# Kernel tuning notes

Hardware: AMD Instinct MI355X
Metric: run time of the kernel (lower is better)

Reference implementation:

```python
import jax, jax.numpy as jnp
import numpy as np

N_A = 500000
N_B = 500000
NUM_HERBS = 25000
D = 128  # hidden_dim


def setup_inputs() -> dict:
    key = jax.random.key(0)
    ks = jax.random.split(key, 12)
    h_A = jax.random.normal(ks[0], (N_A, D), dtype=jnp.float32)
    h_B = jax.random.normal(ks[1], (N_B, D), dtype=jnp.float32)
    herb_idx_A = jnp.sort(jax.random.randint(ks[2], (N_A,), 0, NUM_HERBS, dtype=jnp.int64))
    herb_idx_B = jnp.sort(jax.random.randint(ks[3], (N_B,), 0, NUM_HERBS, dtype=jnp.int64))
    # attn_net: Linear(2D, D//2) -> LeakyReLU(0.2) -> Linear(D//2, 1)
    aw1 = jax.random.normal(ks[4], (2 * D, D // 2), dtype=jnp.float32) / np.sqrt(2 * D)
    ab1 = jnp.zeros((D // 2,), dtype=jnp.float32)
    aw2 = jax.random.normal(ks[5], (D // 2, 1), dtype=jnp.float32) / np.sqrt(D // 2)
    ab2 = jnp.zeros((1,), dtype=jnp.float32)
    # fusion_mlp: Linear(4D, 2D) -> ReLU -> Linear(2D, D)
    fw1 = jax.random.normal(ks[6], (4 * D, 2 * D), dtype=jnp.float32) / np.sqrt(4 * D)
    fb1 = jnp.zeros((2 * D,), dtype=jnp.float32)
    fw2 = jax.random.normal(ks[7], (2 * D, D), dtype=jnp.float32) / np.sqrt(2 * D)
    fb2 = jnp.zeros((D,), dtype=jnp.float32)
    return {"h_A": h_A, "h_B": h_B, "herb_idx_A": herb_idx_A, "herb_idx_B": herb_idx_B,
            "num_herbs": NUM_HERBS,
            "aw1": aw1, "ab1": ab1, "aw2": aw2, "ab2": ab2,
            "fw1": fw1, "fb1": fb1, "fw2": fw2, "fb2": fb2}


def _seg_mean(x, idx, n):
    s = jax.ops.segment_sum(x, idx, num_segments=n)          # [n, D]
    cnt = jax.ops.segment_sum(jnp.ones((x.shape[0], 1), x.dtype), idx, num_segments=n)
    return s / jnp.maximum(cnt, 1.0)


def _seg_softmax(score, idx, n):
    # score: [N, 1]; numerically-stable per-segment softmax (as in PyG softmax)
    m = jax.ops.segment_max(score, idx, num_segments=n)       # [n, 1]
    e = jnp.exp(score - m[idx])
    denom = jax.ops.segment_sum(e, idx, num_segments=n)
    return e / (denom[idx] + 1e-16)


def _attn(x, aw1, ab1, aw2, ab2):
    h = jax.nn.leaky_relu(x @ aw1 + ab1, negative_slope=0.2)
    return h @ aw2 + ab2                                      # [N, 1]


def reference(h_A, h_B, herb_idx_A, herb_idx_B, num_herbs,
              aw1, ab1, aw2, ab2, fw1, fb1, fw2, fb2):
    H_B_mean = _seg_mean(h_B, herb_idx_B, num_herbs)          # [H, D]
    H_A_mean = _seg_mean(h_A, herb_idx_A, num_herbs)          # [H, D]

    cat_A = jnp.concatenate([h_A, H_B_mean[herb_idx_A]], axis=-1)  # [N_A, 2D]
    alpha_A = _seg_softmax(_attn(cat_A, aw1, ab1, aw2, ab2), herb_idx_A, num_herbs)
    H_A_given_B = jax.ops.segment_sum(alpha_A * h_A, herb_idx_A, num_segments=num_herbs)

    cat_B = jnp.concatenate([h_B, H_A_mean[herb_idx_B]], axis=-1)  # [N_B, 2D]
    alpha_B = _seg_softmax(_attn(cat_B, aw1, ab1, aw2, ab2), herb_idx_B, num_herbs)
    H_B_given_A = jax.ops.segment_sum(alpha_B * h_B, herb_idx_B, num_segments=num_herbs)

    concat_feat = jnp.concatenate([H_A_given_B, H_B_given_A,
                                   H_A_given_B * H_B_given_A,
                                   jnp.abs(H_A_given_B - H_B_given_A)], axis=-1)  # [H, 4D]
    H_interaction = jax.nn.relu(concat_feat @ fw1 + fb1) @ fw2 + fb2              # [H, D]
    return (H_interaction, H_A_given_B, H_B_given_A)
```

## Files before the change

kernel.cpp:

```cpp
#include <hip/hip_runtime.h>
#include <math.h>

#define H_HERBS 25000
#define DIM 128

typedef __attribute__((ext_vector_type(8))) short bf16x8;
typedef __attribute__((ext_vector_type(4))) float f32x4;

__device__ inline unsigned pack2bf(float a, float b) {
    union { float f; unsigned u; } x, y; x.f = a; y.f = b;
    return ((x.u + 0x8000u) >> 16) | ((y.u + 0x8000u) & 0xFFFF0000u);
}

__global__ void k_starts(const int* __restrict__ idxA, const int* __restrict__ idxB,
                         int nA, int nB, int* __restrict__ startA, int* __restrict__ startB) {
    int h = blockIdx.x * blockDim.x + threadIdx.x;
    if (h > H_HERBS) return;
    {
        int lo = 0, hi = nA;
        while (lo < hi) { int mid = (lo + hi) >> 1; if (idxA[mid] < h) lo = mid + 1; else hi = mid; }
        startA[h] = lo;
    }
    {
        int lo = 0, hi = nB;
        while (lo < hi) { int mid = (lo + hi) >> 1; if (idxB[mid] < h) lo = mid + 1; else hi = mid; }
        startB[h] = lo;
    }
}

__global__ __launch_bounds__(64) void k_packw(
        const float* __restrict__ fw1, const float* __restrict__ fw2,
        uint4* __restrict__ w1bf, uint4* __restrict__ w2bf) {
    int b = blockIdx.x, l = threadIdx.x;
    int c = l & 15, kg = l >> 4;
    if (b < 256) {
        int kt = b >> 4, nt = b & 15;
        int k0 = kt * 32 + kg * 8, j = nt * 16 + c;
        unsigned u0 = pack2bf(fw1[(size_t)(k0 + 0) * 256 + j], fw1[(size_t)(k0 + 1) * 256 + j]);
        unsigned u1 = pack2bf(fw1[(size_t)(k0 + 2) * 256 + j], fw1[(size_t)(k0 + 3) * 256 + j]);
        unsigned u2 = pack2bf(fw1[(size_t)(k0 + 4) * 256 + j], fw1[(size_t)(k0 + 5) * 256 + j]);
        unsigned u3 = pack2bf(fw1[(size_t)(k0 + 6) * 256 + j], fw1[(size_t)(k0 + 7) * 256 + j]);
        w1bf[(size_t)b * 64 + l] = make_uint4(u0, u1, u2, u3);
    } else {
        int bb = b - 256;
        int kt = bb >> 3, nt = bb & 7;
        int k0 = kt * 32 + kg * 8, j = nt * 16 + c;
        unsigned u0 = pack2bf(fw2[(size_t)(k0 + 0) * 128 + j], fw2[(size_t)(k0 + 1) * 128 + j]);
        unsigned u1 = pack2bf(fw2[(size_t)(k0 + 2) * 128 + j], fw2[(size_t)(k0 + 3) * 128 + j]);
        unsigned u2 = pack2bf(fw2[(size_t)(k0 + 4) * 128 + j], fw2[(size_t)(k0 + 5) * 128 + j]);
        unsigned u3 = pack2bf(fw2[(size_t)(k0 + 6) * 128 + j], fw2[(size_t)(k0 + 7) * 128 + j]);
        w2bf[(size_t)bb * 64 + l] = make_uint4(u0, u1, u2, u3);
    }
}

__global__ __launch_bounds__(256) void k_mean_both(
        const float* __restrict__ hA, const float* __restrict__ hB,
        const int* __restrict__ startA, const int* __restrict__ startB,
        const float* __restrict__ aw1, const float* __restrict__ ab1,
        float* __restrict__ mpartA, float* __restrict__ mpartB, int nhb) {
    __shared__ float Wl[128 * 64];
    __shared__ __align__(16) float mb[16][128];
    bool isA = (int)blockIdx.x < nhb;
    int hb = isA ? blockIdx.x : blockIdx.x - nhb;
    const float* X = isA ? hB : hA;
    const int* start = isA ? startB : startA;
    float* mpart = isA ? mpartA : mpartB;
    int h0 = hb * 16;
    int t = threadIdx.x;

    {
        const float4* Wsrc = (const float4*)(aw1 + 128 * 64);
        float4* Wl4 = (float4*)Wl;
        #pragma unroll
        for (int q = 0; q < 8; ++q) Wl4[t + 256 * q] = Wsrc[t + 256 * q];
    }

    int wv = t >> 6, ln = t & 63, half = ln >> 5, li = ln & 31;
    const float4* X4 = (const float4*)X;
    #pragma unroll
    for (int i = 0; i < 4; ++i) {
        int hh = wv * 4 + i;
        int h = h0 + hh;
        if (h >= H_HERBS) { if (half == 0) ((float4*)mb[hh])[li] = make_float4(0.f,0.f,0.f,0.f); continue; }
        int s = start[h], e = start[h + 1];
        float4 acc = make_float4(0.f, 0.f, 0.f, 0.f);
        int r = s + half;
        for (; r + 6 < e; r += 8) {
            float4 v0 = X4[(size_t)r * 32 + li];
            float4 v1 = X4[(size_t)(r + 2) * 32 + li];
            float4 v2 = X4[(size_t)(r + 4) * 32 + li];
            float4 v3 = X4[(size_t)(r + 6) * 32 + li];
            acc.x += (v0.x + v1.x) + (v2.x + v3.x);
            acc.y += (v0.y + v1.y) + (v2.y + v3.y);
            acc.z += (v0.z + v1.z) + (v2.z + v3.z);
            acc.w += (v0.w + v1.w) + (v2.w + v3.w);
        }
        for (; r < e; r += 2) {
            float4 v0 = X4[(size_t)r * 32 + li];
            acc.x += v0.x; acc.y += v0.y; acc.z += v0.z; acc.w += v0.w;
        }
        acc.x += __shfl_xor(acc.x, 32, 64);
        acc.y += __shfl_xor(acc.y, 32, 64);
        acc.z += __shfl_xor(acc.z, 32, 64);
        acc.w += __shfl_xor(acc.w, 32, 64);
        int cnt = e - s;
        float inv = 1.0f / (float)(cnt > 1 ? cnt : 1);
        if (half == 0) {
            ((float4*)mb[hh])[li] = make_float4(acc.x * inv, acc.y * inv, acc.z * inv, acc.w * inv);
        }
    }
    __syncthreads();

    {
        int j = t & 63, wg = t >> 6;
        float b1 = ab1[j];
        float a0 = b1, a1 = b1, a2 = b1, a3 = b1;
        #pragma unroll 8
        for (int k = 0; k < 128; ++k) {
            float w = Wl[k * 64 + j];
            a0 += mb[wg * 4 + 0][k] * w;
            a1 += mb[wg * 4 + 1][k] * w;
            a2 += mb[wg * 4 + 2][k] * w;
            a3 += mb[wg * 4 + 3][k] * w;
        }
        int h = h0 + wg * 4;
        if (h + 0 < H_HERBS) mpart[(size_t)(h + 0) * 64 + j] = a0;
        if (h + 1 < H_HERBS) mpart[(size_t)(h + 1) * 64 + j] = a1;
        if (h + 2 < H_HERBS) mpart[(size_t)(h + 2) * 64 + j] = a2;
        if (h + 3 < H_HERBS) mpart[(size_t)(h + 3) * 64 + j] = a3;
    }
}

__global__ __launch_bounds__(256) void k_scores_mfma(
        const float* __restrict__ XA, const int* __restrict__ idxA,
        const float* __restrict__ mpartA, int nA, int gridA,
        const float* __restrict__ XB, const int* __restrict__ idxB,
        const float* __restrict__ mpartB, int nB,
        const float* __restrict__ aw1, const float* __restrict__ aw2,
        const float* __restrict__ ab2,
        float* __restrict__ scoresA, float* __restrict__ scoresB) {
    bool isA = (int)blockIdx.x < gridA;
    int blk = isA ? blockIdx.x : blockIdx.x - gridA;
    const float* X = isA ? XA : XB;
    const int* idx = isA ? idxA : idxB;
    const float* mpart = isA ? mpartA : mpartB;
    float* scores = isA ? scoresA : scoresB;
    int n = isA ? nA : nB;

    int t = threadIdx.x;
    int l = t & 63, wid = t >> 6;
    int c = l & 15, kg = l >> 4;

    union ABu { bf16x8 v; unsigned u[4]; };

    ABu wf[4][4];
    #pragma unroll
    for (int kb = 0; kb < 4; ++kb) {
        int k0 = kb * 32 + kg * 8;
        #pragma unroll
        for (int nb = 0; nb < 4; ++nb) {
            int j = nb * 16 + c;
            #pragma unroll
            for (int e = 0; e < 4; ++e) {
                wf[kb][nb].u[e] = pack2bf(aw1[(size_t)(k0 + 2 * e)     * 64 + j],
                                          aw1[(size_t)(k0 + 2 * e + 1) * 64 + j]);
            }
        }
    }
    float a2[4];
    #pragma unroll
    for (int nb = 0; nb < 4; ++nb) a2[nb] = aw2[nb * 16 + c];
    float b2s = ab2[0];

    for (int pass = 0; pass < 4; ++pass) {
        long r0 = (long)blk * 256 + pass * 64 + wid * 16;
        if (r0 >= n) break;
        long myrow = r0 + c;
        if (myrow >= n) myrow = n - 1;
        const float4* Xr = (const float4*)(X + (size_t)myrow * DIM);

        ABu af[4];
        #pragma unroll
        for (int kb = 0; kb < 4; ++kb) {
            float4 a = Xr[kb * 8 + kg * 2];
            float4 b = Xr[kb * 8 + kg * 2 + 1];
            af[kb].u[0] = pack2bf(a.x, a.y);
            af[kb].u[1] = pack2bf(a.z, a.w);
            af[kb].u[2] = pack2bf(b.x, b.y);
            af[kb].u[3] = pack2bf(b.z, b.w);
        }

        f32x4 acc[4];
        #pragma unroll
        for (int nb = 0; nb < 4; ++nb) { acc[nb].x = 0.f; acc[nb].y = 0.f; acc[nb].z = 0.f; acc[nb].w = 0.f; }
        #pragma unroll
        for (int kb = 0; kb < 4; ++kb) {
            #pragma unroll
            for (int nb = 0; nb < 4; ++nb) {
                acc[nb] = __builtin_amdgcn_mfma_f32_16x16x32_bf16(af[kb].v, wf[kb][nb].v, acc[nb], 0, 0, 0);
            }
        }

        int rgrp = kg * 4;
        float part[4] = {0.f, 0.f, 0.f, 0.f};
        #pragma unroll
        for (int reg = 0; reg < 4; ++reg) {
            long rr = r0 + rgrp + reg;
            bool v = rr < n;
            int h = v ? idx[rr] : 0;
            const float* mp = mpart + (size_t)h * 64;
            #pragma unroll
            for (int nb = 0; nb < 4; ++nb) {
                float hv = acc[nb][reg] + mp[nb * 16 + c];
                hv = hv > 0.f ? hv : 0.2f * hv;
                part[reg] += hv * a2[nb];
            }
        }
        #pragma unroll
        for (int reg = 0; reg < 4; ++reg) {
            float p = part[reg];
            p += __shfl_xor(p, 1, 64);
            p += __shfl_xor(p, 2, 64);
            p += __shfl_xor(p, 4, 64);
            p += __shfl_xor(p, 8, 64);
            part[reg] = p;
        }
        if (c == 0) {
            #pragma unroll
            for (int reg = 0; reg < 4; ++reg) {
                long rr = r0 + rgrp + reg;
                if (rr < n) scores[rr] = part[reg] + b2s;
            }
        }
    }
}

__global__ __launch_bounds__(64) void k_attn_both(
        const float* __restrict__ hA, const float* __restrict__ hB,
        const int* __restrict__ startA, const int* __restrict__ startB,
        const float* __restrict__ scoresA, const float* __restrict__ scoresB,
        float* __restrict__ outA, float* __restrict__ outB) {
    int bid = blockIdx.x;
    bool sideA = bid < H_HERBS;
    int h = sideA ? bid : bid - H_HERBS;
    const float* X = sideA ? hA : hB;
    const int* start = sideA ? startA : startB;
    const float* scores = sideA ? scoresA : scoresB;
    float* out = sideA ? outA : outB;

    int lane = threadIdx.x;
    int half = lane >> 5, li = lane & 31;
    int s = start[h], e = start[h + 1];
    const float4* X4 = (const float4*)X;
    float4 acc = make_float4(0.f, 0.f, 0.f, 0.f);
    if (e > s) {
        float mx = -INFINITY;
        for (int r = s + lane; r < e; r += 64) mx = fmaxf(mx, scores[r]);
        #pragma unroll
        for (int o = 32; o; o >>= 1) mx = fmaxf(mx, __shfl_xor(mx, o, 64));
        float sum = 0.f;
        for (int r = s + lane; r < e; r += 64) sum += __expf(scores[r] - mx);
        #pragma unroll
        for (int o = 32; o; o >>= 1) sum += __shfl_xor(sum, o, 64);
        float invden = 1.0f / (sum + 1e-16f);

        int r = s + half;
        for (; r + 6 < e; r += 8) {
            float w0 = __expf(scores[r]     - mx) * invden;
            float w1 = __expf(scores[r + 2] - mx) * invden;
            float w2 = __expf(scores[r + 4] - mx) * invden;
            float w3 = __expf(scores[r + 6] - mx) * invden;
            float4 v0 = X4[(size_t)r * 32 + li];
            float4 v1 = X4[(size_t)(r + 2) * 32 + li];
            float4 v2 = X4[(size_t)(r + 4) * 32 + li];
            float4 v3 = X4[(size_t)(r + 6) * 32 + li];
            acc.x += (w0 * v0.x + w1 * v1.x) + (w2 * v2.x + w3 * v3.x);
            acc.y += (w0 * v0.y + w1 * v1.y) + (w2 * v2.y + w3 * v3.y);
            acc.z += (w0 * v0.z + w1 * v1.z) + (w2 * v2.z + w3 * v3.z);
            acc.w += (w0 * v0.w + w1 * v1.w) + (w2 * v2.w + w3 * v3.w);
        }
        for (; r < e; r += 2) {
            float w0 = __expf(scores[r] - mx) * invden;
            float4 v0 = X4[(size_t)r * 32 + li];
            acc.x += w0 * v0.x; acc.y += w0 * v0.y;
            acc.z += w0 * v0.z; acc.w += w0 * v0.w;
        }
    }
    acc.x += __shfl_xor(acc.x, 32, 64);
    acc.y += __shfl_xor(acc.y, 32, 64);
    acc.z += __shfl_xor(acc.z, 32, 64);
    acc.w += __shfl_xor(acc.w, 32, 64);
    if (half == 0) {
        ((float4*)out)[(size_t)h * 32 + li] = acc;
    }
}

__global__ __launch_bounds__(256) void k_fusion_mfma(
        const float* __restrict__ HA, const float* __restrict__ HB,
        const uint4* __restrict__ w1bf, const uint4* __restrict__ w2bf,
        const float* __restrict__ fb1, const float* __restrict__ fb2,
        float* __restrict__ out) {
    __shared__ float hid[32 * 256];
    int t = threadIdx.x, wid = t >> 6, l = t & 63, c = l & 15, kg = l >> 4;
    int h0 = blockIdx.x * 32;
    int ms = wid & 1, nh = wid >> 1;

    union ABu { bf16x8 v; unsigned u[4]; uint4 q; };

    {
        int rowl = ms * 16 + c;
        int h = h0 + rowl;
        bool hv = h < H_HERBS;
        const float* pa = HA + (size_t)(hv ? h : h0) * DIM;
        const float* pb = HB + (size_t)(hv ? h : h0) * DIM;

        f32x4 acc[8];
        #pragma unroll
        for (int nt = 0; nt < 8; ++nt) { acc[nt].x = 0.f; acc[nt].y = 0.f; acc[nt].z = 0.f; acc[nt].w = 0.f; }

        #pragma unroll
        for (int kt = 0; kt < 16; ++kt) {
            int k0 = kt * 32 + kg * 8;
            int range = k0 >> 7, off = k0 & 127;
            float f[8];
            if (range == 0) {
                float4 a0 = *(const float4*)(pa + off), a1 = *(const float4*)(pa + off + 4);
                f[0] = a0.x; f[1] = a0.y; f[2] = a0.z; f[3] = a0.w;
                f[4] = a1.x; f[5] = a1.y; f[6] = a1.z; f[7] = a1.w;
            } else if (range == 1) {
                float4 b0 = *(const float4*)(pb + off), b1 = *(const float4*)(pb + off + 4);
                f[0] = b0.x; f[1] = b0.y; f[2] = b0.z; f[3] = b0.w;
                f[4] = b1.x; f[5] = b1.y; f[6] = b1.z; f[7] = b1.w;
            } else if (range == 2) {
                float4 a0 = *(const float4*)(pa + off), a1 = *(const float4*)(pa + off + 4);
                float4 b0 = *(const float4*)(pb + off), b1 = *(const float4*)(pb + off + 4);
                f[0] = a0.x * b0.x; f[1] = a0.y * b0.y; f[2] = a0.z * b0.z; f[3] = a0.w * b0.w;
                f[4] = a1.x * b1.x; f[5] = a1.y * b1.y; f[6] = a1.z * b1.z; f[7] = a1.w * b1.w;
            } else {
                float4 a0 = *(const float4*)(pa + off), a1 = *(const float4*)(pa + off + 4);
                float4 b0 = *(const float4*)(pb + off), b1 = *(const float4*)(pb + off + 4);
                f[0] = fabsf(a0.x - b0.x); f[1] = fabsf(a0.y - b0.y);
                f[2] = fabsf(a0.z - b0.z); f[3] = fabsf(a0.w - b0.w);
                f[4] = fabsf(a1.x - b1.x); f[5] = fabsf(a1.y - b1.y);
                f[6] = fabsf(a1.z - b1.z); f[7] = fabsf(a1.w - b1.w);
            }
            ABu af;
            af.u[0] = pack2bf(f[0], f[1]); af.u[1] = pack2bf(f[2], f[3]);
            af.u[2] = pack2bf(f[4], f[5]); af.u[3] = pack2bf(f[6], f[7]);
            #pragma unroll
            for (int nt = 0; nt < 8; ++nt) {
                ABu bfr; bfr.q = w1bf[(size_t)(kt * 16 + nh * 8 + nt) * 64 + l];
                acc[nt] = __builtin_amdgcn_mfma_f32_16x16x32_bf16(af.v, bfr.v, acc[nt], 0, 0, 0);
            }
        }

        #pragma unroll
        for (int nt = 0; nt < 8; ++nt) {
            int j = nh * 128 + nt * 16 + c;
            float b1 = fb1[j];
            #pragma unroll
            for (int reg = 0; reg < 4; ++reg) {
                int row = ms * 16 + kg * 4 + reg;
                float v = fmaxf(acc[nt][reg] + b1, 0.f);
                hid[row * 256 + (j ^ ((row & 7) << 3))] = v;
            }
        }
    }
    __syncthreads();

    {
        int rowl = ms * 16 + c;
        f32x4 acc2[4];
        #pragma unroll
        for (int nt = 0; nt < 4; ++nt) { acc2[nt].x = 0.f; acc2[nt].y = 0.f; acc2[nt].z = 0.f; acc2[nt].w = 0.f; }

        #pragma unroll
        for (int kt = 0; kt < 8; ++kt) {
            int j0 = kt * 32 + kg * 8;
            int widx = rowl * 256 + (j0 ^ ((rowl & 7) << 3));
            float4 h0v = *(const float4*)&hid[widx];
            float4 h1v = *(const float4*)&hid[widx + 4];
            ABu af;
            af.u[0] = pack2bf(h0v.x, h0v.y); af.u[1] = pack2bf(h0v.z, h0v.w);
            af.u[2] = pack2bf(h1v.x, h1v.y); af.u[3] = pack2bf(h1v.z, h1v.w);
            #pragma unroll
            for (int nt = 0; nt < 4; ++nt) {
                ABu bfr; bfr.q = w2bf[(size_t)(kt * 8 + nh * 4 + nt) * 64 + l];
                acc2[nt] = __builtin_amdgcn_mfma_f32_16x16x32_bf16(af.v, bfr.v, acc2[nt], 0, 0, 0);
            }
        }

        #pragma unroll
        for (int nt = 0; nt < 4; ++nt) {
            int j = nh * 64 + nt * 16 + c;
            float b2 = fb2[j];
            #pragma unroll
            for (int reg = 0; reg < 4; ++reg) {
                int row = ms * 16 + kg * 4 + reg;
                int h = h0 + row;
                if (h < H_HERBS) out[(size_t)h * DIM + j] = acc2[nt][reg] + b2;
            }
        }
    }
}

extern "C" void kernel_launch(void* const* d_in, const int* in_sizes, int n_in,
                              void* d_out, int out_size, void* d_ws, size_t ws_size,
                              hipStream_t stream) {
    const float* hA  = (const float*)d_in[0];
    const float* hB  = (const float*)d_in[1];
    const int*   idxA = (const int*)d_in[2];
    const int*   idxB = (const int*)d_in[3];
    const float* aw1 = (const float*)d_in[5];
    const float* ab1 = (const float*)d_in[6];
    const float* aw2 = (const float*)d_in[7];
    const float* ab2 = (const float*)d_in[8];
    const float* fw1 = (const float*)d_in[9];
    const float* fb1 = (const float*)d_in[10];
    const float* fw2 = (const float*)d_in[11];
    const float* fb2 = (const float*)d_in[12];

    int nA = in_sizes[0] / DIM;
    int nB = in_sizes[1] / DIM;

    float* out  = (float*)d_out;
    float* outI = out;
    float* outA = out + (size_t)H_HERBS * DIM;
    float* outB = out + (size_t)2 * H_HERBS * DIM;

    char* w = (char*)d_ws;
    auto carve = [&](size_t bytes) { char* p = w; w += (bytes + 255) & ~(size_t)255; return p; };
    int*   startA  = (int*)carve((size_t)(H_HERBS + 1) * sizeof(int));
    int*   startB  = (int*)carve((size_t)(H_HERBS + 1) * sizeof(int));
    float* mpartA  = (float*)carve((size_t)H_HERBS * 64 * sizeof(float));
    float* mpartB  = (float*)carve((size_t)H_HERBS * 64 * sizeof(float));
    float* scoresA = (float*)carve((size_t)nA * sizeof(float));
    float* scoresB = (float*)carve((size_t)nB * sizeof(float));
    uint4* w1bf    = (uint4*)carve((size_t)256 * 64 * sizeof(uint4));
    uint4* w2bf    = (uint4*)carve((size_t)64 * 64 * sizeof(uint4));

    int gridA = (nA + 255) / 256;
    int gridB = (nB + 255) / 256;

    k_starts<<<(H_HERBS + 1 + 255) / 256, 256, 0, stream>>>(idxA, idxB, nA, nB, startA, startB);

    k_packw<<<320, 64, 0, stream>>>(fw1, fw2, w1bf, w2bf);

    int nhb = (H_HERBS + 15) / 16;
    k_mean_both<<<2 * nhb, 256, 0, stream>>>(hA, hB, startA, startB, aw1, ab1, mpartA, mpartB, nhb);

    k_scores_mfma<<<gridA + gridB, 256, 0, stream>>>(hA, idxA, mpartA, nA, gridA,
                                                     hB, idxB, mpartB, nB,
                                                     aw1, aw2, ab2, scoresA, scoresB);

    k_attn_both<<<2 * H_HERBS, 64, 0, stream>>>(hA, hB, startA, startB, scoresA, scoresB, outA, outB);

    k_fusion_mfma<<<(H_HERBS + 31) / 32, 256, 0, stream>>>(outA, outB, w1bf, w2bf, fb1, fb2, outI);
}
```

Measured before the change: 414.5 us.

## Fuse A-side segment mean into A attention pass and serialize A/B sides

The segment-mean reduction over h_A is now computed inside the A-side attention aggregation kernel, which already streams every h_A row. The mean is written into the interaction output buffer as scratch and then projected by a small new kernel. This removes one full read of h_A (about 256 MB). In exchange, the A and B pipelines run as separate sequential launches instead of combined grids, which adds launches and lowers per-launch parallelism.

```diff
diff --git a/kernel.cpp b/kernel.cpp
--- a/kernel.cpp
+++ b/kernel.cpp
@@ -53,19 +53,13 @@
     }
 }
 
-__global__ __launch_bounds__(256) void k_mean_both(
-        const float* __restrict__ hA, const float* __restrict__ hB,
-        const int* __restrict__ startA, const int* __restrict__ startB,
+__global__ __launch_bounds__(256) void k_mean_proj(
+        const float* __restrict__ X, const int* __restrict__ start,
         const float* __restrict__ aw1, const float* __restrict__ ab1,
-        float* __restrict__ mpartA, float* __restrict__ mpartB, int nhb) {
+        float* __restrict__ mpart) {
     __shared__ float Wl[128 * 64];
     __shared__ __align__(16) float mb[16][128];
-    bool isA = (int)blockIdx.x < nhb;
-    int hb = isA ? blockIdx.x : blockIdx.x - nhb;
-    const float* X = isA ? hB : hA;
-    const int* start = isA ? startB : startA;
-    float* mpart = isA ? mpartA : mpartB;
-    int h0 = hb * 16;
+    int h0 = blockIdx.x * 16;
     int t = threadIdx.x;
 
     {
@@ -131,22 +125,56 @@
     }
 }
 
-__global__ __launch_bounds__(256) void k_scores_mfma(
-        const float* __restrict__ XA, const int* __restrict__ idxA,
-        const float* __restrict__ mpartA, int nA, int gridA,
-        const float* __restrict__ XB, const int* __restrict__ idxB,
-        const float* __restrict__ mpartB, int nB,
+__global__ __launch_bounds__(256) void k_mpart_one(
+        const float* __restrict__ meanG, const float* __restrict__ aw1,
+        const float* __restrict__ ab1, float* __restrict__ mpart) {
+    __shared__ float Wl[128 * 64];
+    __shared__ float mb[64 * 128];
+    int h0 = blockIdx.x * 64;
+    int t = threadIdx.x;
+
+    const float4* Wsrc = (const float4*)(aw1 + 128 * 64);
+    float4* Wl4 = (float4*)Wl;
+    #pragma unroll
+    for (int q = 0; q < 8; ++q) Wl4[t + 256 * q] = Wsrc[t + 256 * q];
+    float4* mb4 = (float4*)mb;
+    const float4* mG4 = (const float4*)meanG;
+    #pragma unroll
+    for (int q = 0; q < 8; ++q) {
+        int ent = t + 256 * q;
+        int hl = ent >> 5, kq = ent & 31;
+        int h = h0 + hl;
+        mb4[ent] = (h < H_HERBS) ? mG4[(size_t)h * 32 + kq] : make_float4(0.f, 0.f, 0.f, 0.f);
+    }
+    __syncthreads();
+
+    int j = t & 63, hg = t >> 6;
+    float b1 = ab1[j];
+    #pragma unroll
+    for (int ii = 0; ii < 4; ++ii) {
+        int hl0 = hg * 16 + ii * 4;
+        float a0 = 0.f, a1 = 0.f, a2 = 0.f, a3 = 0.f;
+        for (int k = 0; k < 128; ++k) {
+            float w = Wl[k * 64 + j];
+            a0 += mb[(hl0 + 0) * 128 + k] * w;
+            a1 += mb[(hl0 + 1) * 128 + k] * w;
+            a2 += mb[(hl0 + 2) * 128 + k] * w;
+            a3 += mb[(hl0 + 3) * 128 + k] * w;
+        }
+        int h = h0 + hl0;
+        if (h + 0 < H_HERBS) mpart[(size_t)(h + 0) * 64 + j] = b1 + a0;
+        if (h + 1 < H_HERBS) mpart[(size_t)(h + 1) * 64 + j] = b1 + a1;
+        if (h + 2 < H_HERBS) mpart[(size_t)(h + 2) * 64 + j] = b1 + a2;
+        if (h + 3 < H_HERBS) mpart[(size_t)(h + 3) * 64 + j] = b1 + a3;
+    }
+}
+
+__global__ __launch_bounds__(256) void k_scores_one(
+        const float* __restrict__ X, const int* __restrict__ idx,
+        const float* __restrict__ mpart,
         const float* __restrict__ aw1, const float* __restrict__ aw2,
         const float* __restrict__ ab2,
-        float* __restrict__ scoresA, float* __restrict__ scoresB) {
-    bool isA = (int)blockIdx.x < gridA;
-    int blk = isA ? blockIdx.x : blockIdx.x - gridA;
-    const float* X = isA ? XA : XB;
-    const int* idx = isA ? idxA : idxB;
-    const float* mpart = isA ? mpartA : mpartB;
-    float* scores = isA ? scoresA : scoresB;
-    int n = isA ? nA : nB;
-
+        float* __restrict__ scores, int n) {
     int t = threadIdx.x;
     int l = t & 63, wid = t >> 6;
     int c = l & 15, kg = l >> 4;
@@ -173,7 +201,7 @@
     float b2s = ab2[0];
 
     for (int pass = 0; pass < 4; ++pass) {
-        long r0 = (long)blk * 256 + pass * 64 + wid * 16;
+        long r0 = (long)blockIdx.x * 256 + pass * 64 + wid * 16;
         if (r0 >= n) break;
         long myrow = r0 + c;
         if (myrow >= n) myrow = n - 1;
@@ -235,24 +263,18 @@
     }
 }
 
-__global__ __launch_bounds__(64) void k_attn_both(
-        const float* __restrict__ hA, const float* __restrict__ hB,
-        const int* __restrict__ startA, const int* __restrict__ startB,
-        const float* __restrict__ scoresA, const float* __restrict__ scoresB,
-        float* __restrict__ outA, float* __restrict__ outB) {
-    int bid = blockIdx.x;
-    bool sideA = bid < H_HERBS;
-    int h = sideA ? bid : bid - H_HERBS;
-    const float* X = sideA ? hA : hB;
-    const int* start = sideA ? startA : startB;
-    const float* scores = sideA ? scoresA : scoresB;
-    float* out = sideA ? outA : outB;
-
+template <bool WITH_MEAN>
+__global__ __launch_bounds__(64) void k_attn_one(
+        const float* __restrict__ X, const int* __restrict__ start,
+        const float* __restrict__ scores,
+        float* __restrict__ out, float* __restrict__ meanOut) {
+    int h = blockIdx.x;
     int lane = threadIdx.x;
     int half = lane >> 5, li = lane & 31;
     int s = start[h], e = start[h + 1];
     const float4* X4 = (const float4*)X;
     float4 acc = make_float4(0.f, 0.f, 0.f, 0.f);
+    float4 accS = make_float4(0.f, 0.f, 0.f, 0.f);
     if (e > s) {
         float mx = -INFINITY;
         for (int r = s + lane; r < e; r += 64) mx = fmaxf(mx, scores[r]);
@@ -278,20 +300,41 @@
             acc.y += (w0 * v0.y + w1 * v1.y) + (w2 * v2.y + w3 * v3.y);
             acc.z += (w0 * v0.z + w1 * v1.z) + (w2 * v2.z + w3 * v3.z);
             acc.w += (w0 * v0.w + w1 * v1.w) + (w2 * v2.w + w3 * v3.w);
+            if (WITH_MEAN) {
+                accS.x += (v0.x + v1.x) + (v2.x + v3.x);
+                accS.y += (v0.y + v1.y) + (v2.y + v3.y);
+                accS.z += (v0.z + v1.z) + (v2.z + v3.z);
+                accS.w += (v0.w + v1.w) + (v2.w + v3.w);
+            }
         }
         for (; r < e; r += 2) {
             float w0 = __expf(scores[r] - mx) * invden;
             float4 v0 = X4[(size_t)r * 32 + li];
             acc.x += w0 * v0.x; acc.y += w0 * v0.y;
             acc.z += w0 * v0.z; acc.w += w0 * v0.w;
+            if (WITH_MEAN) {
+                accS.x += v0.x; accS.y += v0.y; accS.z += v0.z; accS.w += v0.w;
+            }
         }
     }
     acc.x += __shfl_xor(acc.x, 32, 64);
     acc.y += __shfl_xor(acc.y, 32, 64);
     acc.z += __shfl_xor(acc.z, 32, 64);
     acc.w += __shfl_xor(acc.w, 32, 64);
+    if (WITH_MEAN) {
+        accS.x += __shfl_xor(accS.x, 32, 64);
+        accS.y += __shfl_xor(accS.y, 32, 64);
+        accS.z += __shfl_xor(accS.z, 32, 64);
+        accS.w += __shfl_xor(accS.w, 32, 64);
+    }
     if (half == 0) {
         ((float4*)out)[(size_t)h * 32 + li] = acc;
+        if (WITH_MEAN) {
+            int cnt = e - s;
+            float inv = 1.0f / (float)(cnt > 1 ? cnt : 1);
+            ((float4*)meanOut)[(size_t)h * 32 + li] =
+                make_float4(accS.x * inv, accS.y * inv, accS.z * inv, accS.w * inv);
+        }
     }
 }
 
@@ -427,6 +470,7 @@
     float* outI = out;
     float* outA = out + (size_t)H_HERBS * DIM;
     float* outB = out + (size_t)2 * H_HERBS * DIM;
+    float* meanA = outI;
 
     char* w = (char*)d_ws;
     auto carve = [&](size_t bytes) { char* p = w; w += (bytes + 255) & ~(size_t)255; return p; };
@@ -441,19 +485,17 @@
 
     int gridA = (nA + 255) / 256;
     int gridB = (nB + 255) / 256;
+    int nhb16 = (H_HERBS + 15) / 16;
+    int nhb64 = (H_HERBS + 63) / 64;
 
     k_starts<<<(H_HERBS + 1 + 255) / 256, 256, 0, stream>>>(idxA, idxB, nA, nB, startA, startB);
-
     k_packw<<<320, 64, 0, stream>>>(fw1, fw2, w1bf, w2bf);
 
-    int nhb = (H_HERBS + 15) / 16;
-    k_mean_both<<<2 * nhb, 256, 0, stream>>>(hA, hB, startA, startB, aw1, ab1, mpartA, mpartB, nhb);
-
-    k_scores_mfma<<<gridA + gridB, 256, 0, stream>>>(hA, idxA, mpartA, nA, gridA,
-                                                     hB, idxB, mpartB, nB,
-                                                     aw1, aw2, ab2, scoresA, scoresB);
-
-    k_attn_both<<<2 * H_HERBS, 64, 0, stream>>>(hA, hB, startA, startB, scoresA, scoresB, outA, outB);
-
+    k_mean_proj<<<nhb16, 256, 0, stream>>>(hB, startB, aw1, ab1, mpartA);
+    k_scores_one<<<gridA, 256, 0, stream>>>(hA, idxA, mpartA, aw1, aw2, ab2, scoresA, nA);
+    k_attn_one<true><<<H_HERBS, 64, 0, stream>>>(hA, startA, scoresA, outA, meanA);
+    k_mpart_one<<<nhb64, 256, 0, stream>>>(meanA, aw1, ab1, mpartB);
+    k_scores_one<<<gridB, 256, 0, stream>>>(hB, idxB, mpartB, aw1, aw2, ab2, scoresB, nB);
+    k_attn_one<false><<<H_HERBS, 64, 0, stream>>>(hB, startB, scoresB, outB, nullptr);
     k_fusion_mfma<<<(H_HERBS + 31) / 32, 256, 0, stream>>>(outA, outB, w1bf, w2bf, fb1, fb2, outI);
 }
```

Result: faster. 388.1 us (-6.4%).
